# Performance work log

Hardware: AMD Instinct MI355X
Metric: run time of the kernel (lower is better)

The kernel has to match this reference:

```python
import jax, jax.numpy as jnp
import numpy as np

N_KNN = 16
BN_EPS = 1e-5


def conv1d(x, w, b):
    # x: (B,Cin,N), w: (Cout,Cin) -> (B,Cout,N)
    return jnp.einsum('oc,bcn->bon', w, x) + b[None, :, None]


def conv2d(x, w, b):
    # x: (B,Cin,N,K), w: (Cout,Cin) -> (B,Cout,N,K)
    return jnp.einsum('oc,bcnk->bonk', w, x) + b[None, :, None, None]


def bn2d(x, gamma, beta):
    # training-mode BatchNorm2d over (B,N,K) per channel
    mu = x.mean(axis=(0, 2, 3), keepdims=True)
    var = x.var(axis=(0, 2, 3), keepdims=True)
    return (x - mu) * jax.lax.rsqrt(var + BN_EPS) * gamma[None, :, None, None] + beta[None, :, None, None]


def knn_idx(pos, k):
    # pos: (B,3,N) -> (B,N,K) indices of k nearest neighbors (include_self=True)
    p = jnp.transpose(pos, (0, 2, 1))  # (B,N,3)
    sq = jnp.sum(p * p, axis=-1)  # (B,N)
    d = sq[:, :, None] + sq[:, None, :] - 2.0 * jnp.einsum('bnd,bmd->bnm', p, p)
    _, idx = jax.lax.top_k(-d, k)
    return idx


def group(feat, idx):
    # feat: (B,C,N), idx: (B,N,K) -> (B,C,N,K)
    return jnp.take_along_axis(feat[:, :, :, None], idx[:, None, :, :], axis=2)


def mlp_res(x, w1, b1, w2, b2, wsc, bsc):
    shortcut = conv1d(x, wsc, bsc)
    return conv1d(jax.nn.relu(conv1d(x, w1, b1)), w2, b2) + shortcut


def setup_inputs() -> dict:
    key0 = jax.random.key(0)
    ks = jax.random.split(key0, 16)
    B, N, C, D, PH = 2, 2048, 128, 256, 64
    AH = D * 4
    f = lambda i, shape: jax.random.normal(ks[i], shape, jnp.float32) * 0.02
    return dict(
        pos=jax.random.normal(ks[0], (B, 3, N), jnp.float32),
        key=jax.random.normal(ks[1], (B, C, N), jnp.float32),
        query=jax.random.normal(ks[2], (B, C, N), jnp.float32),
        mlp_w1=f(3, (C, 2 * C)), mlp_b1=jnp.zeros(C),
        mlp_w2=f(4, (C, C)), mlp_b2=jnp.zeros(C),
        mlp_wsc=f(5, (C, 2 * C)), mlp_bsc=jnp.zeros(C),
        wk=f(6, (D, C)), bk=jnp.zeros(D),
        wq=f(7, (D, C)), bq=jnp.zeros(D),
        wv=f(8, (D, C)), bv=jnp.zeros(D),
        pos_w1=f(9, (PH, 3)), pos_b1=jnp.zeros(PH),
        pos_g=jnp.ones(PH), pos_beta=jnp.zeros(PH),
        pos_w2=f(10, (D, PH)), pos_b2=jnp.zeros(D),
        attn_w1=f(11, (AH, D)), attn_b1=jnp.zeros(AH),
        attn_g=jnp.ones(AH), attn_beta=jnp.zeros(AH),
        attn_w2=f(12, (D, AH)), attn_b2=jnp.zeros(D),
        end_w=f(13, (C, D)), end_b=jnp.zeros(C),
    )


def reference(pos, key, query,
              mlp_w1, mlp_b1, mlp_w2, mlp_b2, mlp_wsc, mlp_bsc,
              wk, bk, wq, bq, wv, bv,
              pos_w1, pos_b1, pos_g, pos_beta, pos_w2, pos_b2,
              attn_w1, attn_b1, attn_g, attn_beta, attn_w2, attn_b2,
              end_w, end_b):
    # value = MLP_Res(cat(key, query))
    value = mlp_res(jnp.concatenate([key, query], axis=1),
                    mlp_w1, mlp_b1, mlp_w2, mlp_b2, mlp_wsc, mlp_bsc)
    identity = value
    k = conv1d(key, wk, bk)      # (B,D,N)
    q = conv1d(query, wq, bq)    # (B,D,N)
    v = conv1d(value, wv, bv)    # (B,D,N)

    idx = knn_idx(pos, N_KNN)    # (B,N,K)
    key_g = group(k, idx)        # (B,D,N,K)
    qk_rel = q[:, :, :, None] - key_g
    pos_rel = pos[:, :, :, None] - group(pos, idx)  # (B,3,N,K)

    # pos_mlp: conv2d -> BN -> ReLU -> conv2d
    h = jax.nn.relu(bn2d(conv2d(pos_rel, pos_w1, pos_b1), pos_g, pos_beta))
    pos_emb = conv2d(h, pos_w2, pos_b2)  # (B,D,N,K)

    # attn_mlp: conv2d -> BN -> ReLU -> conv2d, softmax over neighbor axis
    a = jax.nn.relu(bn2d(conv2d(qk_rel + pos_emb, attn_w1, attn_b1), attn_g, attn_beta))
    attn = jax.nn.softmax(conv2d(a, attn_w2, attn_b2), axis=-1)  # (B,D,N,K)

    val = v[:, :, :, None] + pos_emb
    agg = jnp.sum(attn * val, axis=-1)  # (B,D,N)
    y = conv1d(agg, end_w, end_b)
    return y + identity
```

## Files before the change

kernel.cpp:

```cpp
#include <hip/hip_runtime.h>
#include <hip/hip_bf16.h>
#include <math.h>

#define Bv 2
#define Nv 2048
#define Cv 128
#define Dv 256
#define PHv 64
#define AHv 1024
#define Kv 16
#define NSAMP (Bv*Nv*Kv)

typedef unsigned short ushortt;
typedef unsigned char u8;
typedef __attribute__((ext_vector_type(8))) short bf16x8;
typedef __attribute__((ext_vector_type(4))) float f32x4;

__device__ __forceinline__ float bf2f(ushortt h){
  union { unsigned int u; float f; } v; v.u = ((unsigned int)h) << 16; return v.f;
}
__device__ __forceinline__ ushortt f2bf(float f){
  union { unsigned int u; float f; } v; v.f = f;
  unsigned int r = v.u + 0x7FFFu + ((v.u >> 16) & 1u);
  return (ushortt)(r >> 16);
}
__device__ __forceinline__ u8 f2fp8(float f){
  union { float f; unsigned int u; } v; v.f = f;
  unsigned int s = (v.u >> 24) & 0x80u;
  unsigned int a = v.u & 0x7FFFFFFFu;
  if (a > 0x43E00000u) a = 0x43E00000u;
  unsigned int r = a + 0x7FFFFu + ((a >> 20) & 1u);
  int e = (int)((r >> 23) & 0xFF) - 120;
  unsigned int m = (r >> 20) & 7u;
  if (e <= 0) return (u8)s;
  return (u8)(s | ((unsigned)e << 3) | m);
}
__device__ __forceinline__ u8 f2fp8u(float f){
  union { float f; unsigned int u; } v; v.f = f;
  unsigned int a = v.u;
  if (a > 0x43E00000u) a = 0x43E00000u;
  unsigned int r = a + 0x7FFFFu + ((a >> 20) & 1u);
  unsigned int out = (r >> 20) - 960u;
  return (u8)(r < 0x3C800000u ? 0u : out);
}

__device__ __forceinline__ void gload16(const void* g, void* l){
  __builtin_amdgcn_global_load_lds(
      (const __attribute__((address_space(1))) unsigned int*)g,
      (__attribute__((address_space(3))) unsigned int*)l, 16, 0, 0);
}

__global__ __launch_bounds__(256) void prep_kernel(
    const float* __restrict__ wk, const float* __restrict__ wq,
    const float* __restrict__ wv, const float* __restrict__ endw,
    const float* __restrict__ mw1, const float* __restrict__ mw2,
    const float* __restrict__ mwsc, const float* __restrict__ aw2,
    const float* __restrict__ pw2,
    const float* __restrict__ key, const float* __restrict__ query,
    ushortt* __restrict__ wA16, ushortt* __restrict__ wB16, ushortt* __restrict__ wv16,
    float* __restrict__ endwT, u8* __restrict__ w2f8, ushortt* __restrict__ pw2R,
    ushortt* __restrict__ hx16)
{
  __shared__ float xs[256*33];
  int t = threadIdx.x;
  if (blockIdx.x < 128){
    int tile = blockIdx.x & 63, b = blockIdx.x >> 6;
    int n0 = tile*32;
    for (int e = t; e < 256*32; e += 256){
      int c = e >> 5, nn = e & 31;
      xs[c*33+nn] = (c < 128) ? key[(size_t)(b*128+c)*Nv + n0+nn]
                              : query[(size_t)(b*128+(c-128))*Nv + n0+nn];
    }
    __syncthreads();
    int nn = t & 31, cg = t >> 5;
    size_t s = (size_t)b*Nv + n0 + nn;
    __align__(16) ushortt tmp[32];
    #pragma unroll
    for (int cc = 0; cc < 32; cc++) tmp[cc] = f2bf(xs[(cg*32+cc)*33 + nn]);
    uint4* dst = (uint4*)&hx16[s*384 + 128 + cg*32];
    #pragma unroll
    for (int q = 0; q < 4; q++) dst[q] = ((uint4*)tmp)[q];
    return;
  }
  int tid = (blockIdx.x-128)*256 + t;
  int stride = (gridDim.x-128)*256;
  for (int i = tid; i < 768*256; i += stride){
    int r = i >> 8, c = i & 255;
    float v;
    if (r < 128) v = mw1[r*256 + c];
    else if (r < 384) v = (c < 128) ? wk[(r-128)*128 + c] : 0.f;
    else if (r < 640) v = (c >= 128) ? wq[(r-384)*128 + (c-128)] : 0.f;
    else v = 0.f;
    wA16[i] = f2bf(v);
  }
  for (int i = tid; i < 128*384; i += stride){
    int r = i / 384, c = i - r*384;
    float v = (c < 128) ? mw2[r*128 + c] : mwsc[r*256 + (c-128)];
    wB16[i] = f2bf(v);
  }
  for (int i = tid; i < 256*128; i += stride) wv16[i] = f2bf(wv[i]);
  for (int i = tid; i < 128*256; i += stride){ int co = i>>8, d = i&255; endwT[d*128+co] = endw[i]; }
  for (int i = tid; i < 256*1024; i += stride) w2f8[i] = f2fp8(aw2[i]*256.f);
  for (int i = tid; i < 256*64; i += stride) pw2R[i] = f2bf(pw2[i]);
}

__global__ __launch_bounds__(512) void gemmA_kernel(
    ushortt* __restrict__ hx16, const ushortt* __restrict__ wA16,
    const float* __restrict__ mb1, const float* __restrict__ bk, const float* __restrict__ bq,
    float* __restrict__ kT, float* __restrict__ qT)
{
  __shared__ ushortt As[128*64];
  __shared__ ushortt Bs[256*64];
  int t = threadIdx.x;
  int w = t >> 6, l = t & 63;
  int lr = l & 15, g4 = l >> 4;
  int wm = w >> 2, wn = w & 3;
  int s0 = blockIdx.x*128, n0 = blockIdx.y*256;

  f32x4 acc[4][4];
  #pragma unroll
  for (int i=0;i<4;i++) for (int j=0;j<4;j++) acc[i][j] = (f32x4){0.f,0.f,0.f,0.f};

  for (int kt = 0; kt < 4; kt++){
    int k0 = kt*64;
    __syncthreads();
    #pragma unroll
    for (int i = 0; i < 2; i++){
      int c = t + i*512;
      int r = c >> 3, db = (c & 7)*16;
      const ushortt* src = hx16 + (size_t)(s0+r)*384 + 128 + k0 + ((db ^ ((r&7)<<4))>>1);
      gload16(src, As + c*8);
    }
    #pragma unroll
    for (int i = 0; i < 4; i++){
      int c = t + i*512;
      int r = c >> 3, db = (c & 7)*16;
      const ushortt* src = wA16 + (size_t)(n0+r)*256 + k0 + ((db ^ ((r&7)<<4))>>1);
      gload16(src, Bs + c*8);
    }
    __syncthreads();
    #pragma unroll
    for (int kk = 0; kk < 2; kk++){
      int kb = kk*64 + g4*16;
      bf16x8 af[4];
      #pragma unroll
      for (int mi = 0; mi < 4; mi++){
        int row = wm*64 + mi*16 + lr;
        af[mi] = *(const bf16x8*)((const char*)As + row*128 + (kb ^ ((row&7)<<4)));
      }
      #pragma unroll
      for (int ni = 0; ni < 4; ni++){
        int row = wn*64 + ni*16 + lr;
        bf16x8 bfr = *(const bf16x8*)((const char*)Bs + row*128 + (kb ^ ((row&7)<<4)));
        #pragma unroll
        for (int mi = 0; mi < 4; mi++)
          acc[mi][ni] = __builtin_amdgcn_mfma_f32_16x16x32_bf16(af[mi], bfr, acc[mi][ni], 0,0,0);
      }
    }
  }
  #pragma unroll
  for (int ni = 0; ni < 4; ni++){
    int col = n0 + wn*64 + ni*16 + lr;
    if (col < 128){
      float bias = mb1[col];
      #pragma unroll
      for (int mi = 0; mi < 4; mi++){
        int rbase = s0 + wm*64 + mi*16 + g4*4;
        #pragma unroll
        for (int r = 0; r < 4; r++){
          float v = acc[mi][ni][r] + bias;
          v = v > 0.f ? v : 0.f;
          hx16[(size_t)(rbase+r)*384 + col] = f2bf(v);
        }
      }
    } else if (col < 384){
      float bias = bk[col-128];
      #pragma unroll
      for (int mi = 0; mi < 4; mi++){
        int rbase = s0 + wm*64 + mi*16 + g4*4;
        #pragma unroll
        for (int r = 0; r < 4; r++)
          kT[(size_t)(rbase+r)*256 + (col-128)] = acc[mi][ni][r] + bias;
      }
    } else if (col < 640){
      float bias = bq[col-384];
      #pragma unroll
      for (int mi = 0; mi < 4; mi++){
        int rbase = s0 + wm*64 + mi*16 + g4*4;
        #pragma unroll
        for (int r = 0; r < 4; r++)
          qT[(size_t)(rbase+r)*256 + (col-384)] = acc[mi][ni][r] + bias;
      }
    }
  }
}

__global__ __launch_bounds__(512) void gemmBC_kernel(
    const ushortt* __restrict__ hx16, const ushortt* __restrict__ wB16,
    const float* __restrict__ mb2, const float* __restrict__ mbsc,
    const ushortt* __restrict__ wv16, const float* __restrict__ bv,
    float* __restrict__ valueT, float* __restrict__ vT)
{
  __shared__ char arena[65536];
  ushortt* As = (ushortt*)arena;
  ushortt* Bs = (ushortt*)(arena + 16384);
  ushortt* Ws = (ushortt*)arena;
  char*    Vs = arena + 32768;
  int t = threadIdx.x;
  int w = t >> 6, l = t & 63;
  int lr = l & 15, g4 = l >> 4;
  int wm = w >> 2, wn = w & 3;
  int s0 = blockIdx.x*128;

  {
    f32x4 acc[4][2];
    #pragma unroll
    for (int i=0;i<4;i++) for (int j=0;j<2;j++) acc[i][j] = (f32x4){0.f,0.f,0.f,0.f};

    for (int kt = 0; kt < 6; kt++){
      int k0 = kt*64;
      __syncthreads();
      #pragma unroll
      for (int i = 0; i < 2; i++){
        int c = t + i*512;
        int r = c >> 3, db = (c & 7)*16;
        const ushortt* src = hx16 + (size_t)(s0+r)*384 + k0 + ((db ^ ((r&7)<<4))>>1);
        gload16(src, As + c*8);
      }
      #pragma unroll
      for (int i = 0; i < 2; i++){
        int c = t + i*512;
        int r = c >> 3, db = (c & 7)*16;
        const ushortt* src = wB16 + (size_t)r*384 + k0 + ((db ^ ((r&7)<<4))>>1);
        gload16(src, Bs + c*8);
      }
      __syncthreads();
      #pragma unroll
      for (int kk = 0; kk < 2; kk++){
        int kb = kk*64 + g4*16;
        bf16x8 af[4];
        #pragma unroll
        for (int mi = 0; mi < 4; mi++){
          int row = wm*64 + mi*16 + lr;
          af[mi] = *(const bf16x8*)((const char*)As + row*128 + (kb ^ ((row&7)<<4)));
        }
        #pragma unroll
        for (int ni = 0; ni < 2; ni++){
          int row = wn*32 + ni*16 + lr;
          bf16x8 bfr = *(const bf16x8*)((const char*)Bs + row*128 + (kb ^ ((row&7)<<4)));
          #pragma unroll
          for (int mi = 0; mi < 4; mi++)
            acc[mi][ni] = __builtin_amdgcn_mfma_f32_16x16x32_bf16(af[mi], bfr, acc[mi][ni], 0,0,0);
        }
      }
    }
    #pragma unroll
    for (int ni = 0; ni < 2; ni++){
      int col = wn*32 + ni*16 + lr;
      float bias = mb2[col] + mbsc[col];
      #pragma unroll
      for (int mi = 0; mi < 4; mi++){
        int rloc = wm*64 + mi*16 + g4*4;
        #pragma unroll
        for (int r = 0; r < 4; r++){
          float v = acc[mi][ni][r] + bias;
          valueT[(size_t)(s0+rloc+r)*128 + col] = v;
          int row = rloc + r;
          *(ushortt*)(Vs + row*256 + ((col*2) ^ ((row&7)<<4))) = f2bf(v);
        }
      }
    }
  }
  {
    f32x4 acc2[4][4];
    #pragma unroll
    for (int i=0;i<4;i++) for (int j=0;j<4;j++) acc2[i][j] = (f32x4){0.f,0.f,0.f,0.f};

    for (int kt = 0; kt < 2; kt++){
      int k0 = kt*64;
      __syncthreads();
      #pragma unroll
      for (int i = 0; i < 4; i++){
        int c = t + i*512;
        int r = c >> 3, db = (c & 7)*16;
        const ushortt* src = wv16 + (size_t)r*128 + k0 + ((db ^ ((r&7)<<4))>>1);
        gload16(src, Ws + c*8);
      }
      __syncthreads();
      #pragma unroll
      for (int kk = 0; kk < 2; kk++){
        int kb = kk*64 + g4*16;
        bf16x8 af[4];
        #pragma unroll
        for (int mi = 0; mi < 4; mi++){
          int row = wm*64 + mi*16 + lr;
          af[mi] = *(const bf16x8*)(Vs + row*256 + ((kt*128 + kb) ^ ((row&7)<<4)));
        }
        #pragma unroll
        for (int ni = 0; ni < 4; ni++){
          int row = wn*64 + ni*16 + lr;
          bf16x8 bfr = *(const bf16x8*)((const char*)Ws + row*128 + (kb ^ ((row&7)<<4)));
          #pragma unroll
          for (int mi = 0; mi < 4; mi++)
            acc2[mi][ni] = __builtin_amdgcn_mfma_f32_16x16x32_bf16(af[mi], bfr, acc2[mi][ni], 0,0,0);
        }
      }
    }
    #pragma unroll
    for (int ni = 0; ni < 4; ni++){
      int col = wn*64 + ni*16 + lr;
      float bias = bv[col];
      #pragma unroll
      for (int mi = 0; mi < 4; mi++){
        int rbase = s0 + wm*64 + mi*16 + g4*4;
        #pragma unroll
        for (int r = 0; r < 4; r++)
          vT[(size_t)(rbase+r)*256 + col] = acc2[mi][ni][r] + bias;
      }
    }
  }
}

__global__ __launch_bounds__(256) void knn_kernel(const float* __restrict__ pos, int* __restrict__ idx)
{
  int t = threadIdx.x;
  int w = t >> 6, l = t & 63;
  int p = blockIdx.x*4 + w;
  int i = p & (Nv-1), b = p >> 11;
  const float* px = pos + (size_t)b*3*Nv;
  float pix = px[i], piy = px[Nv+i], piz = px[2*Nv+i];
  float sqi = pix*pix + piy*piy + piz*piz;
  float ds[32];
  #pragma unroll
  for (int jj = 0; jj < 32; jj++){
    int j = jj*64 + l;
    float qx = px[j], qy = px[Nv+j], qz = px[2*Nv+j];
    float sqj = qx*qx + qy*qy + qz*qz;
    float dot = pix*qx + piy*qy + piz*qz;
    ds[jj] = (sqi + sqj) - 2.0f*dot;
  }
  #pragma unroll 1
  for (int it = 0; it < 16; it++){
    float bv = 3.4e38f; int bj = 0x7FFFFFFF;
    #pragma unroll
    for (int jj = 0; jj < 32; jj++){
      int j = jj*64 + l;
      bool c = ds[jj] < bv;
      bv = c ? ds[jj] : bv;
      bj = c ? j : bj;
    }
    #pragma unroll
    for (int off = 32; off; off >>= 1){
      float ov = __shfl_xor(bv, off);
      int oj = __shfl_xor(bj, off);
      if (ov < bv || (ov == bv && oj < bj)){ bv = ov; bj = oj; }
    }
    if (l == 0) idx[(size_t)p*16 + it] = bj;
    #pragma unroll
    for (int jj = 0; jj < 32; jj++){
      if (jj*64 + l == bj) ds[jj] = 3.4e38f;
    }
  }
}

__global__ __launch_bounds__(256) void bn1_stats(const float* __restrict__ pos,
    const int* __restrict__ idx, float* __restrict__ rstat)
{
  int tid = blockIdx.x*256 + threadIdx.x;
  int stride = gridDim.x*256;
  float s[9] = {0,0,0,0,0,0,0,0,0};
  for (int e = tid; e < NSAMP; e += stride){
    int b = e >> 15;
    int rem = e & 32767;
    int n = rem >> 4, k = rem & 15;
    int j = idx[(size_t)(b*Nv+n)*16 + k];
    const float* px = pos + (size_t)b*3*Nv;
    float rx = px[n]-px[j], ry = px[Nv+n]-px[Nv+j], rz = px[2*Nv+n]-px[2*Nv+j];
    s[0]+=rx; s[1]+=ry; s[2]+=rz;
    s[3]+=rx*rx; s[4]+=rx*ry; s[5]+=rx*rz; s[6]+=ry*ry; s[7]+=ry*rz; s[8]+=rz*rz;
  }
  for (int off=32; off; off>>=1)
    for (int q=0;q<9;q++) s[q] += __shfl_xor(s[q], off);
  if ((threadIdx.x & 63) == 0)
    for (int q=0;q<9;q++) atomicAdd(&rstat[q], s[q]);
}

__global__ __launch_bounds__(256) void hpos_kernel(
    const float* __restrict__ pos, const int* __restrict__ idx,
    const float* __restrict__ rstat, const float* __restrict__ pw1,
    const float* __restrict__ pg, const float* __restrict__ pbeta,
    ushortt* __restrict__ hposR)
{
  __shared__ float w1s[192];
  __shared__ float b1s[64];
  int t = threadIdx.x;
  if (t < 64){
    float inv = 1.0f/(float)NSAMP;
    float mux = rstat[0]*inv, muy = rstat[1]*inv, muz = rstat[2]*inv;
    float xx = rstat[3]*inv, xy = rstat[4]*inv, xz = rstat[5]*inv;
    float yy = rstat[6]*inv, yz = rstat[7]*inv, zz = rstat[8]*inv;
    float w0 = pw1[t*3], w1 = pw1[t*3+1], w2 = pw1[t*3+2];
    float dot = w0*mux + w1*muy + w2*muz;
    float quad = w0*w0*xx + w1*w1*yy + w2*w2*zz + 2.f*(w0*w1*xy + w0*w2*xz + w1*w2*yz);
    float var = quad - dot*dot;
    float sc = pg[t] * rsqrtf(var + 1e-5f);
    w1s[t*3]   = w0*sc;
    w1s[t*3+1] = w1*sc;
    w1s[t*3+2] = w2*sc;
    b1s[t] = pbeta[t] - dot*sc;
  }
  __syncthreads();
  int s = blockIdx.x*32 + (t>>3);
  int c0 = (t&7)*8;
  int ptv = s >> 4;
  int n = ptv & (Nv-1), b = ptv >> 11;
  int j = idx[s];
  const float* px = pos + (size_t)b*3*Nv;
  float rx = px[n]-px[j], ry = px[Nv+n]-px[Nv+j], rz = px[2*Nv+n]-px[2*Nv+j];
  ushortt outv[8];
  #pragma unroll
  for (int e = 0; e < 8; e++){
    int c = c0+e;
    float v = b1s[c] + w1s[c*3]*rx + w1s[c*3+1]*ry + w1s[c*3+2]*rz;
    outv[e] = f2bf(v > 0.f ? v : 0.f);
  }
  *(uint4*)&hposR[(size_t)s*64 + c0] = *(uint4*)outv;
}

__global__ __launch_bounds__(512) void gemm0_kernel(
    const ushortt* __restrict__ hposR, const ushortt* __restrict__ pw2R,
    const float* __restrict__ pb2, const int* __restrict__ idx,
    const float* __restrict__ qT, const float* __restrict__ kT, const float* __restrict__ vT,
    ushortt* __restrict__ U16, ushortt* __restrict__ val16, float* __restrict__ mu_sum)
{
  __shared__ ushortt As[128*64];
  __shared__ ushortt Bs[256*64];
  __shared__ float mured[8*256];
  int t = threadIdx.x;
  int w = t >> 6, l = t & 63;
  int lr = l & 15, g4 = l >> 4;
  int wm = w >> 2, wn = w & 3;
  int s0 = blockIdx.x*128;

  #pragma unroll
  for (int i = 0; i < 2; i++){
    int c = t + i*512;
    int r = c >> 3, db = (c & 7)*16;
    const ushortt* src = hposR + (size_t)(s0+r)*64 + ((db ^ ((r&7)<<4))>>1);
    gload16(src, As + c*8);
  }
  #pragma unroll
  for (int i = 0; i < 4; i++){
    int c = t + i*512;
    int r = c >> 3, db = (c & 7)*16;
    const ushortt* src = pw2R + (size_t)r*64 + ((db ^ ((r&7)<<4))>>1);
    gload16(src, Bs + c*8);
  }
  __syncthreads();

  f32x4 acc[4][4];
  #pragma unroll
  for (int i=0;i<4;i++) for (int j=0;j<4;j++) acc[i][j] = (f32x4){0.f,0.f,0.f,0.f};
  #pragma unroll
  for (int kk = 0; kk < 2; kk++){
    int kb = kk*64 + g4*16;
    bf16x8 af[4];
    #pragma unroll
    for (int mi = 0; mi < 4; mi++){
      int row = wm*64 + mi*16 + lr;
      af[mi] = *(const bf16x8*)((const char*)As + row*128 + (kb ^ ((row&7)<<4)));
    }
    #pragma unroll
    for (int ni = 0; ni < 4; ni++){
      int row = wn*64 + ni*16 + lr;
      bf16x8 bfr = *(const bf16x8*)((const char*)Bs + row*128 + (kb ^ ((row&7)<<4)));
      #pragma unroll
      for (int mi = 0; mi < 4; mi++)
        acc[mi][ni] = __builtin_amdgcn_mfma_f32_16x16x32_bf16(af[mi], bfr, acc[mi][ni], 0,0,0);
    }
  }

  float musum[4] = {0.f,0.f,0.f,0.f};
  __align__(16) float pb2v[4];
  #pragma unroll
  for (int ni = 0; ni < 4; ni++) pb2v[ni] = pb2[wn*64 + ni*16 + lr];
  #pragma unroll
  for (int mi = 0; mi < 4; mi++){
    #pragma unroll
    for (int r4 = 0; r4 < 4; r4++){
      int s = s0 + wm*64 + mi*16 + g4*4 + r4;
      int ptv = s >> 4;
      int b = s >> 15;
      int j = idx[s];
      const float* krow = kT + (size_t)(b*Nv + j)*256;
      const float* qrow = qT + (size_t)ptv*256;
      const float* vrow = vT + (size_t)ptv*256;
      #pragma unroll
      for (int ni = 0; ni < 4; ni++){
        int d = wn*64 + ni*16 + lr;
        float pe = acc[mi][ni][r4] + pb2v[ni];
        float u = qrow[d] - krow[d] + pe;
        U16[(size_t)s*256 + d] = f2bf(u);
        val16[(size_t)s*256 + d] = f2bf(vrow[d] + pe);
        musum[ni] += u;
      }
    }
  }
  #pragma unroll
  for (int ni = 0; ni < 4; ni++)
    mured[(wm*4+g4)*256 + wn*64 + ni*16 + lr] = musum[ni];
  __syncthreads();
  if (t < 256){
    float ssum = 0.f;
    #pragma unroll
    for (int q = 0; q < 8; q++) ssum += mured[q*256 + t];
    atomicAdd(&mu_sum[t], ssum);
  }
}

__global__ __launch_bounds__(512) void mm_kernel(const ushortt* __restrict__ U16,
                                                 ushortt* __restrict__ Mpart)
{
  __shared__ ushortt Ut[256*64];
  int t = threadIdx.x;
  int w = t >> 6, l = t & 63;
  int lr = l & 15, g4 = l >> 4;
  int wm = w >> 2, wn = w & 3;
  int c_my = ((w & 3)*64 + l);
  int sg = w >> 2;
  int blk = blockIdx.x;
  int sstart = blk*256;

  f32x4 acc[8][4];
  #pragma unroll
  for (int i=0;i<8;i++) for (int j=0;j<4;j++) acc[i][j] = (f32x4){0.f,0.f,0.f,0.f};

  for (int st = 0; st < 4; st++){
    int sb = sstart + st*64;
    __syncthreads();
    #pragma unroll
    for (int g = 0; g < 4; g++){
      int s8 = sg*32 + g*8;
      ushortt vals[8];
      #pragma unroll
      for (int e = 0; e < 8; e++)
        vals[e] = U16[(size_t)(sb + s8 + e)*256 + c_my];
      unsigned int p0 = (unsigned int)vals[0] | ((unsigned int)vals[1] << 16);
      unsigned int p1 = (unsigned int)vals[2] | ((unsigned int)vals[3] << 16);
      unsigned int p2 = (unsigned int)vals[4] | ((unsigned int)vals[5] << 16);
      unsigned int p3 = (unsigned int)vals[6] | ((unsigned int)vals[7] << 16);
      uint4 pk = make_uint4(p0,p1,p2,p3);
      *(uint4*)((char*)Ut + c_my*128 + ((s8*2) ^ ((c_my&7)<<4))) = pk;
    }
    __syncthreads();
    #pragma unroll
    for (int kk = 0; kk < 2; kk++){
      int kb = kk*64 + g4*16;
      bf16x8 af[8];
      #pragma unroll
      for (int ci = 0; ci < 8; ci++){
        int row = wm*128 + ci*16 + lr;
        af[ci] = *(const bf16x8*)((const char*)Ut + row*128 + (kb ^ ((row&7)<<4)));
      }
      #pragma unroll
      for (int cj = 0; cj < 4; cj++){
        int row = wn*64 + cj*16 + lr;
        bf16x8 bfr = *(const bf16x8*)((const char*)Ut + row*128 + (kb ^ ((row&7)<<4)));
        #pragma unroll
        for (int ci = 0; ci < 8; ci++)
          acc[ci][cj] = __builtin_amdgcn_mfma_f32_16x16x32_bf16(af[ci], bfr, acc[ci][cj], 0,0,0);
      }
    }
  }
  ushortt* dst = Mpart + (size_t)blk*65536;
  #pragma unroll
  for (int ci = 0; ci < 8; ci++){
    #pragma unroll
    for (int cj = 0; cj < 4; cj++){
      int c2 = wn*64 + cj*16 + lr;
      #pragma unroll
      for (int r = 0; r < 4; r++){
        int c1 = wm*128 + ci*16 + g4*4 + r;
        dst[(size_t)c1*256 + c2] = f2bf(acc[ci][cj][r]);
      }
    }
  }
}

__global__ __launch_bounds__(256) void mreduce_kernel(const ushortt* __restrict__ Mpart,
                                                      float* __restrict__ Mm)
{
  int i = blockIdx.x*256 + threadIdx.x;
  float s = 0.f;
  for (int p = 0; p < 256; p++) s += bf2f(Mpart[(size_t)p*65536 + i]);
  Mm[i] = s;
}

__global__ __launch_bounds__(256) void bn2_final(
    const float* __restrict__ Mm, const float* __restrict__ mu_sum,
    const float* __restrict__ aw1,
    const float* __restrict__ ag, const float* __restrict__ abeta,
    ushortt* __restrict__ w1R, float* __restrict__ b1eff2)
{
  __shared__ float wrow[256];
  __shared__ float red[8];
  __shared__ float s2s;
  int t = threadIdx.x;
  int ch = blockIdx.x;
  wrow[t] = aw1[(size_t)ch*256 + t];
  __syncthreads();
  float colacc = 0.f;
  for (int r = 0; r < 256; r++) colacc += wrow[r] * Mm[(size_t)r*256 + t];
  float inv = 1.0f/(float)NSAMP;
  float qpart = colacc * wrow[t] * inv;
  float dpart = wrow[t] * mu_sum[t] * inv;
  for (int off=32; off; off>>=1){ qpart += __shfl_xor(qpart, off); dpart += __shfl_xor(dpart, off); }
  if ((t&63)==0){ red[t>>6] = qpart; red[4 + (t>>6)] = dpart; }
  __syncthreads();
  if (t == 0){
    float quad = red[0]+red[1]+red[2]+red[3];
    float dot  = red[4]+red[5]+red[6]+red[7];
    float var = quad - dot*dot;
    float s2 = ag[ch] * rsqrtf(var + 1e-5f);
    b1eff2[ch] = abeta[ch] - dot*s2;
    s2s = s2;
  }
  __syncthreads();
  w1R[(size_t)ch*256 + t] = f2bf(wrow[t]*s2s);
}

__global__ __launch_bounds__(512) void gemm1_kernel(
    const ushortt* __restrict__ U16c, const ushortt* __restrict__ w1R,
    const float* __restrict__ b1eff2, u8* __restrict__ H)
{
  __shared__ ushortt As[128*64];
  __shared__ ushortt Bs[256*64];
  int t = threadIdx.x;
  int w = t >> 6, l = t & 63;
  int lr = l & 15, g4 = l >> 4;
  int wm = w >> 2, wn = w & 3;
  int nwg = gridDim.x, cpx = nwg >> 3;
  int logical = (blockIdx.x & 7)*cpx + (blockIdx.x >> 3);
  int mt = logical >> 2, nt = logical & 3;
  int s0 = mt*128, n0 = nt*256;

  f32x4 acc[4][4];
  #pragma unroll
  for (int i=0;i<4;i++) for (int j=0;j<4;j++) acc[i][j] = (f32x4){0.f,0.f,0.f,0.f};

  for (int kt = 0; kt < 4; kt++){
    int k0 = kt*64;
    __syncthreads();
    #pragma unroll
    for (int i = 0; i < 2; i++){
      int c = t + i*512;
      int r = c >> 3, db = (c & 7)*16;
      const ushortt* src = U16c + (size_t)(s0+r)*256 + k0 + ((db ^ ((r&7)<<4))>>1);
      gload16(src, As + c*8);
    }
    #pragma unroll
    for (int i = 0; i < 4; i++){
      int c = t + i*512;
      int r = c >> 3, db = (c & 7)*16;
      const ushortt* src = w1R + (size_t)(n0+r)*256 + k0 + ((db ^ ((r&7)<<4))>>1);
      gload16(src, Bs + c*8);
    }
    __syncthreads();
    #pragma unroll
    for (int kk = 0; kk < 2; kk++){
      int kb = kk*64 + g4*16;
      bf16x8 af[4];
      #pragma unroll
      for (int mi = 0; mi < 4; mi++){
        int row = wm*64 + mi*16 + lr;
        af[mi] = *(const bf16x8*)((const char*)As + row*128 + (kb ^ ((row&7)<<4)));
      }
      #pragma unroll
      for (int ni = 0; ni < 4; ni++){
        int row = wn*64 + ni*16 + lr;
        bf16x8 bfr = *(const bf16x8*)((const char*)Bs + row*128 + (kb ^ ((row&7)<<4)));
        #pragma unroll
        for (int mi = 0; mi < 4; mi++)
          acc[mi][ni] = __builtin_amdgcn_mfma_f32_16x16x32_bf16(af[mi], bfr, acc[mi][ni], 0,0,0);
      }
    }
  }
  __syncthreads();
  u8* rep = (u8*)Bs;
  #pragma unroll
  for (int ni = 0; ni < 4; ni++){
    int colc = wn*64 + ni*16 + lr;
    float bias = b1eff2[n0 + colc];
    #pragma unroll
    for (int mi = 0; mi < 4; mi++){
      int sloc = wm*64 + mi*16 + g4*4;
      #pragma unroll
      for (int r = 0; r < 4; r++){
        float v = acc[mi][ni][r] + bias;
        v = v > 0.f ? v : 0.f;
        rep[(sloc+r)*256 + colc] = f2fp8u(4.f*v);
      }
    }
  }
  __syncthreads();
  #pragma unroll
  for (int i = 0; i < 4; i++){
    int e = t + i*512;
    int row = e >> 4, off = (e & 15)*16;
    *(uint4*)&H[(size_t)(s0+row)*1024 + n0 + off] = *(const uint4*)(rep + e*16);
  }
}

__global__ __launch_bounds__(512) void gemm2_kernel(
    const u8* __restrict__ H, const u8* __restrict__ w2f8,
    const float* __restrict__ ab2, const ushortt* __restrict__ val16,
    float* __restrict__ aggT, int s_off)
{
  __shared__ u8 As8[128*128];
  __shared__ u8 Bs8[256*128];
  int t = threadIdx.x;
  int w = t >> 6, l = t & 63;
  int lr = l & 15, g4 = l >> 4;
  int wm = w >> 2, wn = w & 3;
  int blk = blockIdx.x;
  int s0 = blk*128;

  f32x4 acc[4][4];
  #pragma unroll
  for (int i=0;i<4;i++) for (int j=0;j<4;j++) acc[i][j] = (f32x4){0.f,0.f,0.f,0.f};

  for (int kt = 0; kt < 8; kt++){
    int k0 = kt*128;
    __syncthreads();
    #pragma unroll
    for (int i = 0; i < 2; i++){
      int c = t + i*512;
      int r = c >> 3, db = (c & 7)*16;
      const u8* src = H + (size_t)(s0+r)*1024 + k0 + (db ^ ((r&7)<<4));
      gload16(src, As8 + c*16);
    }
    #pragma unroll
    for (int i = 0; i < 4; i++){
      int c = t + i*512;
      int r = c >> 3, db = (c & 7)*16;
      const u8* src = w2f8 + (size_t)r*1024 + k0 + (db ^ ((r&7)<<4));
      gload16(src, Bs8 + c*16);
    }
    __syncthreads();
    #pragma unroll
    for (int kk = 0; kk < 4; kk++){
      int kb = kk*32 + g4*8;
      long af[4];
      #pragma unroll
      for (int mi = 0; mi < 4; mi++){
        int row = wm*64 + mi*16 + lr;
        af[mi] = *(const long*)(As8 + row*128 + (kb ^ ((row&7)<<4)));
      }
      #pragma unroll
      for (int ni = 0; ni < 4; ni++){
        int row = wn*64 + ni*16 + lr;
        long bfr = *(const long*)(Bs8 + row*128 + (kb ^ ((row&7)<<4)));
        #pragma unroll
        for (int mi = 0; mi < 4; mi++)
          acc[mi][ni] = __builtin_amdgcn_mfma_f32_16x16x32_fp8_fp8(af[mi], bfr, acc[mi][ni], 0,0,0);
      }
    }
  }
  const float sc = 1.0f/1024.0f;
  int ptbase = s_off >> 4;
  #pragma unroll
  for (int mi = 0; mi < 4; mi++){
    int pt = ptbase + blk*8 + wm*4 + mi;
    int sbase = pt*16;
    #pragma unroll
    for (int ni = 0; ni < 4; ni++){
      int d = wn*64 + ni*16 + lr;
      float bias = ab2[d];
      float lg[4];
      #pragma unroll
      for (int r = 0; r < 4; r++) lg[r] = acc[mi][ni][r]*sc + bias;
      float mx = fmaxf(fmaxf(lg[0],lg[1]), fmaxf(lg[2],lg[3]));
      mx = fmaxf(mx, __shfl_xor(mx, 16));
      mx = fmaxf(mx, __shfl_xor(mx, 32));
      float ev[4], ss = 0.f;
      #pragma unroll
      for (int r = 0; r < 4; r++){ ev[r] = __expf(lg[r]-mx); ss += ev[r]; }
      ss += __shfl_xor(ss, 16);
      ss += __shfl_xor(ss, 32);
      float inv = 1.0f/ss;
      float pa = 0.f;
      #pragma unroll
      for (int r = 0; r < 4; r++){
        int s = sbase + g4*4 + r;
        pa += ev[r]*inv*bf2f(val16[(size_t)s*256 + d]);
      }
      pa += __shfl_xor(pa, 16);
      pa += __shfl_xor(pa, 32);
      if (g4 == 0) aggT[(size_t)pt*256 + d] = pa;
    }
  }
}

__global__ __launch_bounds__(256) void final_kernel(
    const float* __restrict__ aggT, const float* __restrict__ endwT,
    const float* __restrict__ endb, const float* __restrict__ valueT,
    float* __restrict__ out)
{
  __shared__ float ags[32*257];
  int t = threadIdx.x;
  int tile = blockIdx.x & 63, b = blockIdx.x >> 6;
  int n0 = tile*32;
  for (int e = t; e < 32*256; e += 256){
    int nn = e >> 8, d = e & 255;
    ags[nn*257 + d] = aggT[(size_t)(b*Nv + n0 + nn)*256 + d];
  }
  __syncthreads();
  int cg = t >> 2, ng = t & 3;
  int co0 = cg*2, nb = ng*8;
  float acc[2][8];
  for (int i=0;i<2;i++){ float bb = endb[co0+i]; for (int j=0;j<8;j++) acc[i][j]=bb; }
  for (int d = 0; d < 256; d++){
    float w0 = endwT[d*128 + co0], w1 = endwT[d*128 + co0 + 1];
    #pragma unroll
    for (int j=0;j<8;j++){
      float av = ags[(nb+j)*257 + d];
      acc[0][j] += w0*av; acc[1][j] += w1*av;
    }
  }
  for (int i=0;i<2;i++){
    for (int j=0;j<8;j++){
      int n = n0 + nb + j;
      size_t o = (size_t)(b*128 + co0 + i)*Nv + n;
      out[o] = acc[i][j] + valueT[(size_t)(b*Nv + n)*128 + co0 + i];
    }
  }
}

extern "C" void kernel_launch(void* const* d_in, const int* in_sizes, int n_in,
                              void* d_out, int out_size, void* d_ws, size_t ws_size,
                              hipStream_t stream)
{
  (void)in_sizes; (void)n_in; (void)out_size;
  const float* pos   = (const float*)d_in[0];
  const float* key   = (const float*)d_in[1];
  const float* query = (const float*)d_in[2];
  const float* mw1   = (const float*)d_in[3];
  const float* mb1   = (const float*)d_in[4];
  const float* mw2   = (const float*)d_in[5];
  const float* mb2   = (const float*)d_in[6];
  const float* mwsc  = (const float*)d_in[7];
  const float* mbsc  = (const float*)d_in[8];
  const float* wk    = (const float*)d_in[9];
  const float* bk    = (const float*)d_in[10];
  const float* wq    = (const float*)d_in[11];
  const float* bq    = (const float*)d_in[12];
  const float* wv    = (const float*)d_in[13];
  const float* bv    = (const float*)d_in[14];
  const float* pw1   = (const float*)d_in[15];
  const float* pg    = (const float*)d_in[17];
  const float* pbeta = (const float*)d_in[18];
  const float* pw2   = (const float*)d_in[19];
  const float* pb2   = (const float*)d_in[20];
  const float* aw1   = (const float*)d_in[21];
  const float* ag    = (const float*)d_in[23];
  const float* abeta = (const float*)d_in[24];
  const float* aw2   = (const float*)d_in[25];
  const float* ab2   = (const float*)d_in[26];
  const float* endw  = (const float*)d_in[27];
  const float* endb  = (const float*)d_in[28];
  float* out = (float*)d_out;

  char* wsb = (char*)d_ws;
  size_t off = 0;
  auto take = [&](size_t bytes)->char*{
    char* p = wsb + off; off += (bytes + 255) & ~(size_t)255; return p;
  };
  float* Mm      = (float*)take(65536*4);
  float* mu_sum  = (float*)take(256*4);
  float* rstat   = (float*)take(12*4);
  size_t zero_bytes = off;
  float* b1eff2  = (float*)take(1024*4);
  float* valueT  = (float*)take((size_t)524288*4);
  float* qT      = (float*)take((size_t)1048576*4);
  float* kT      = (float*)take((size_t)1048576*4);
  float* vT      = (float*)take((size_t)1048576*4);
  float* aggT    = (float*)take((size_t)1048576*4);
  float* endwT   = (float*)take(32768*4);
  int*   idxb    = (int*)take(65536*4);
  ushortt* hx16  = (ushortt*)take((size_t)4096*384*2);
  ushortt* wA16  = (ushortt*)take((size_t)768*256*2);
  ushortt* wB16  = (ushortt*)take((size_t)128*384*2);
  ushortt* wv16  = (ushortt*)take((size_t)256*128*2);
  ushortt* U16   = (ushortt*)take((size_t)16777216*2);
  ushortt* val16 = (ushortt*)take((size_t)16777216*2);
  ushortt* hposR = (ushortt*)take((size_t)4194304*2);
  ushortt* Mpart = (ushortt*)take((size_t)256*65536*2);
  ushortt* w1R   = (ushortt*)take((size_t)262144*2);
  u8*      w2f8  = (u8*)take((size_t)262144);
  ushortt* pw2R  = (ushortt*)take(16384*2);

  size_t avail = (ws_size > off) ? (ws_size - off) : 0;
  int nch = 1;
  while (nch < 64 && ((size_t)(NSAMP/nch))*1024 > avail) nch <<= 1;
  int chunk = NSAMP / nch;
  u8* H = (u8*)(wsb + off);

  hipMemsetAsync(d_ws, 0, zero_bytes, stream);
  prep_kernel<<<640,256,0,stream>>>(wk,wq,wv,endw,mw1,mw2,mwsc,aw2,pw2,key,query,
                                    wA16,wB16,wv16,endwT,w2f8,pw2R,hx16);
  knn_kernel<<<1024,256,0,stream>>>(pos,idxb);
  gemmA_kernel<<<dim3(32,3),512,0,stream>>>(hx16,wA16,mb1,bk,bq,kT,qT);
  gemmBC_kernel<<<32,512,0,stream>>>(hx16,wB16,mb2,mbsc,wv16,bv,valueT,vT);
  bn1_stats<<<64,256,0,stream>>>(pos,idxb,rstat);
  hpos_kernel<<<2048,256,0,stream>>>(pos,idxb,rstat,pw1,pg,pbeta,hposR);
  gemm0_kernel<<<512,512,0,stream>>>(hposR,pw2R,pb2,idxb,qT,kT,vT,U16,val16,mu_sum);
  mm_kernel<<<256,512,0,stream>>>(U16,Mpart);
  mreduce_kernel<<<256,256,0,stream>>>(Mpart,Mm);
  bn2_final<<<1024,256,0,stream>>>(Mm,mu_sum,aw1,ag,abeta,w1R,b1eff2);
  for (int cc = 0; cc < nch; cc++){
    int s_off = cc*chunk;
    gemm1_kernel<<<(chunk/128)*4,512,0,stream>>>(U16 + (size_t)s_off*256, w1R, b1eff2, H);
    gemm2_kernel<<<chunk/128,512,0,stream>>>(H, w2f8, ab2, val16, aggT, s_off);
  }
  final_kernel<<<128,256,0,stream>>>(aggT,endwT,endb,valueT,out);
}
```

Baseline: 280.9 us.

## Fuse attention MLP GEMM1 and GEMM2 keeping hidden activations in LDS

Merges the two attention-MLP GEMMs into one kernel. Each block computes its 128-sample hidden tile in 256-column chunks, quantizes it to fp8 in shared memory, and feeds it straight into the second GEMM with the softmax/aggregation epilogue. This removes the large fp8 H round trip through global memory and the chunked launch loop. In exchange, each block recomputes over all four N tiles serially, so there is less parallelism per launch (512 blocks instead of 2048+512) and shared memory use grows to 64KB, which lowers occupancy.

New measurement: 357.7 us. 27.3% more time.

```diff
diff --git a/kernel.cpp b/kernel.cpp
--- a/kernel.cpp
+++ b/kernel.cpp
@@ -629,148 +629,123 @@
   w1R[(size_t)ch*256 + t] = f2bf(wrow[t]*s2s);
 }
 
-__global__ __launch_bounds__(512) void gemm1_kernel(
-    const ushortt* __restrict__ U16c, const ushortt* __restrict__ w1R,
-    const float* __restrict__ b1eff2, u8* __restrict__ H)
-{
-  __shared__ ushortt As[128*64];
-  __shared__ ushortt Bs[256*64];
+__global__ __launch_bounds__(512) void gemm12_kernel(
+    const ushortt* __restrict__ U16, const ushortt* __restrict__ w1R,
+    const float* __restrict__ b1eff2, const u8* __restrict__ w2f8,
+    const float* __restrict__ ab2, const ushortt* __restrict__ val16,
+    float* __restrict__ aggT)
+{
+  __shared__ char arena[65536];
+  ushortt* As  = (ushortt*)arena;
+  ushortt* Bs1 = (ushortt*)(arena + 16384);
+  u8* Hs  = (u8*)arena;
+  u8* W2s = (u8*)(arena + 32768);
   int t = threadIdx.x;
   int w = t >> 6, l = t & 63;
   int lr = l & 15, g4 = l >> 4;
   int wm = w >> 2, wn = w & 3;
   int nwg = gridDim.x, cpx = nwg >> 3;
-  int logical = (blockIdx.x & 7)*cpx + (blockIdx.x >> 3);
-  int mt = logical >> 2, nt = logical & 3;
-  int s0 = mt*128, n0 = nt*256;
-
-  f32x4 acc[4][4];
-  #pragma unroll
-  for (int i=0;i<4;i++) for (int j=0;j<4;j++) acc[i][j] = (f32x4){0.f,0.f,0.f,0.f};
-
-  for (int kt = 0; kt < 4; kt++){
-    int k0 = kt*64;
+  int mt = (blockIdx.x & 7)*cpx + (blockIdx.x >> 3);
+  int s0 = mt*128;
+
+  f32x4 acc2[4][4];
+  #pragma unroll
+  for (int i=0;i<4;i++) for (int j=0;j<4;j++) acc2[i][j] = (f32x4){0.f,0.f,0.f,0.f};
+
+  for (int nt = 0; nt < 4; nt++){
+    int n0 = nt*256;
+    f32x4 acc1[4][4];
+    #pragma unroll
+    for (int i=0;i<4;i++) for (int j=0;j<4;j++) acc1[i][j] = (f32x4){0.f,0.f,0.f,0.f};
+    for (int kt = 0; kt < 4; kt++){
+      int k0 = kt*64;
+      __syncthreads();
+      #pragma unroll
+      for (int i = 0; i < 2; i++){
+        int c = t + i*512;
+        int r = c >> 3, db = (c & 7)*16;
+        const ushortt* src = U16 + (size_t)(s0+r)*256 + k0 + ((db ^ ((r&7)<<4))>>1);
+        gload16(src, As + c*8);
+      }
+      #pragma unroll
+      for (int i = 0; i < 4; i++){
+        int c = t + i*512;
+        int r = c >> 3, db = (c & 7)*16;
+        const ushortt* src = w1R + (size_t)(n0+r)*256 + k0 + ((db ^ ((r&7)<<4))>>1);
+        gload16(src, Bs1 + c*8);
+      }
+      __syncthreads();
+      #pragma unroll
+      for (int kk = 0; kk < 2; kk++){
+        int kb = kk*64 + g4*16;
+        bf16x8 af[4];
+        #pragma unroll
+        for (int mi = 0; mi < 4; mi++){
+          int row = wm*64 + mi*16 + lr;
+          af[mi] = *(const bf16x8*)((const char*)As + row*128 + (kb ^ ((row&7)<<4)));
+        }
+        #pragma unroll
+        for (int ni = 0; ni < 4; ni++){
+          int row = wn*64 + ni*16 + lr;
+          bf16x8 bfr = *(const bf16x8*)((const char*)Bs1 + row*128 + (kb ^ ((row&7)<<4)));
+          #pragma unroll
+          for (int mi = 0; mi < 4; mi++)
+            acc1[mi][ni] = __builtin_amdgcn_mfma_f32_16x16x32_bf16(af[mi], bfr, acc1[mi][ni], 0,0,0);
+        }
+      }
+    }
     __syncthreads();
     #pragma unroll
-    for (int i = 0; i < 2; i++){
-      int c = t + i*512;
-      int r = c >> 3, db = (c & 7)*16;
-      const ushortt* src = U16c + (size_t)(s0+r)*256 + k0 + ((db ^ ((r&7)<<4))>>1);
-      gload16(src, As + c*8);
-    }
-    #pragma unroll
-    for (int i = 0; i < 4; i++){
-      int c = t + i*512;
-      int r = c >> 3, db = (c & 7)*16;
-      const ushortt* src = w1R + (size_t)(n0+r)*256 + k0 + ((db ^ ((r&7)<<4))>>1);
-      gload16(src, Bs + c*8);
-    }
-    __syncthreads();
-    #pragma unroll
-    for (int kk = 0; kk < 2; kk++){
-      int kb = kk*64 + g4*16;
-      bf16x8 af[4];
+    for (int ni = 0; ni < 4; ni++){
+      int colc = wn*64 + ni*16 + lr;
+      float bias = b1eff2[n0 + colc];
       #pragma unroll
       for (int mi = 0; mi < 4; mi++){
-        int row = wm*64 + mi*16 + lr;
-        af[mi] = *(const bf16x8*)((const char*)As + row*128 + (kb ^ ((row&7)<<4)));
-      }
-      #pragma unroll
-      for (int ni = 0; ni < 4; ni++){
-        int row = wn*64 + ni*16 + lr;
-        bf16x8 bfr = *(const bf16x8*)((const char*)Bs + row*128 + (kb ^ ((row&7)<<4)));
-        #pragma unroll
-        for (int mi = 0; mi < 4; mi++)
-          acc[mi][ni] = __builtin_amdgcn_mfma_f32_16x16x32_bf16(af[mi], bfr, acc[mi][ni], 0,0,0);
-      }
-    }
-  }
-  __syncthreads();
-  u8* rep = (u8*)Bs;
-  #pragma unroll
-  for (int ni = 0; ni < 4; ni++){
-    int colc = wn*64 + ni*16 + lr;
-    float bias = b1eff2[n0 + colc];
-    #pragma unroll
-    for (int mi = 0; mi < 4; mi++){
-      int sloc = wm*64 + mi*16 + g4*4;
-      #pragma unroll
-      for (int r = 0; r < 4; r++){
-        float v = acc[mi][ni][r] + bias;
-        v = v > 0.f ? v : 0.f;
-        rep[(sloc+r)*256 + colc] = f2fp8u(4.f*v);
-      }
-    }
-  }
-  __syncthreads();
-  #pragma unroll
-  for (int i = 0; i < 4; i++){
-    int e = t + i*512;
-    int row = e >> 4, off = (e & 15)*16;
-    *(uint4*)&H[(size_t)(s0+row)*1024 + n0 + off] = *(const uint4*)(rep + e*16);
-  }
-}
-
-__global__ __launch_bounds__(512) void gemm2_kernel(
-    const u8* __restrict__ H, const u8* __restrict__ w2f8,
-    const float* __restrict__ ab2, const ushortt* __restrict__ val16,
-    float* __restrict__ aggT, int s_off)
-{
-  __shared__ u8 As8[128*128];
-  __shared__ u8 Bs8[256*128];
-  int t = threadIdx.x;
-  int w = t >> 6, l = t & 63;
-  int lr = l & 15, g4 = l >> 4;
-  int wm = w >> 2, wn = w & 3;
-  int blk = blockIdx.x;
-  int s0 = blk*128;
-
-  f32x4 acc[4][4];
-  #pragma unroll
-  for (int i=0;i<4;i++) for (int j=0;j<4;j++) acc[i][j] = (f32x4){0.f,0.f,0.f,0.f};
-
-  for (int kt = 0; kt < 8; kt++){
-    int k0 = kt*128;
-    __syncthreads();
-    #pragma unroll
-    for (int i = 0; i < 2; i++){
-      int c = t + i*512;
-      int r = c >> 3, db = (c & 7)*16;
-      const u8* src = H + (size_t)(s0+r)*1024 + k0 + (db ^ ((r&7)<<4));
-      gload16(src, As8 + c*16);
-    }
-    #pragma unroll
-    for (int i = 0; i < 4; i++){
-      int c = t + i*512;
-      int r = c >> 3, db = (c & 7)*16;
-      const u8* src = w2f8 + (size_t)r*1024 + k0 + (db ^ ((r&7)<<4));
-      gload16(src, Bs8 + c*16);
-    }
-    __syncthreads();
-    #pragma unroll
-    for (int kk = 0; kk < 4; kk++){
-      int kb = kk*32 + g4*8;
-      long af[4];
-      #pragma unroll
-      for (int mi = 0; mi < 4; mi++){
-        int row = wm*64 + mi*16 + lr;
-        af[mi] = *(const long*)(As8 + row*128 + (kb ^ ((row&7)<<4)));
-      }
-      #pragma unroll
-      for (int ni = 0; ni < 4; ni++){
-        int row = wn*64 + ni*16 + lr;
-        long bfr = *(const long*)(Bs8 + row*128 + (kb ^ ((row&7)<<4)));
-        #pragma unroll
-        for (int mi = 0; mi < 4; mi++)
-          acc[mi][ni] = __builtin_amdgcn_mfma_f32_16x16x32_fp8_fp8(af[mi], bfr, acc[mi][ni], 0,0,0);
-      }
+        int sloc = wm*64 + mi*16 + g4*4;
+        #pragma unroll
+        for (int r = 0; r < 4; r++){
+          float v = acc1[mi][ni][r] + bias;
+          v = v > 0.f ? v : 0.f;
+          int row = sloc + r;
+          Hs[row*256 + (colc ^ ((row&7)<<4))] = f2fp8u(4.f*v);
+        }
+      }
+    }
+    #pragma unroll
+    for (int sub = 0; sub < 2; sub++){
+      #pragma unroll
+      for (int i = 0; i < 4; i++){
+        int c = t + i*512;
+        int r = c >> 3, db = (c & 7)*16;
+        const u8* src = w2f8 + (size_t)r*1024 + n0 + sub*128 + (db ^ ((r&7)<<4));
+        gload16(src, W2s + c*16);
+      }
+      __syncthreads();
+      #pragma unroll
+      for (int kk = 0; kk < 4; kk++){
+        int kb = kk*32 + g4*8;
+        long af[4];
+        #pragma unroll
+        for (int mi = 0; mi < 4; mi++){
+          int row = wm*64 + mi*16 + lr;
+          af[mi] = *(const long*)(Hs + row*256 + ((sub*128 + kb) ^ ((row&7)<<4)));
+        }
+        #pragma unroll
+        for (int ni = 0; ni < 4; ni++){
+          int row = wn*64 + ni*16 + lr;
+          long bfr = *(const long*)(W2s + row*128 + (kb ^ ((row&7)<<4)));
+          #pragma unroll
+          for (int mi = 0; mi < 4; mi++)
+            acc2[mi][ni] = __builtin_amdgcn_mfma_f32_16x16x32_fp8_fp8(af[mi], bfr, acc2[mi][ni], 0,0,0);
+        }
+      }
+      __syncthreads();
     }
   }
   const float sc = 1.0f/1024.0f;
-  int ptbase = s_off >> 4;
   #pragma unroll
   for (int mi = 0; mi < 4; mi++){
-    int pt = ptbase + blk*8 + wm*4 + mi;
+    int pt = mt*8 + wm*4 + mi;
     int sbase = pt*16;
     #pragma unroll
     for (int ni = 0; ni < 4; ni++){
@@ -778,7 +753,7 @@
       float bias = ab2[d];
       float lg[4];
       #pragma unroll
-      for (int r = 0; r < 4; r++) lg[r] = acc[mi][ni][r]*sc + bias;
+      for (int r = 0; r < 4; r++) lg[r] = acc2[mi][ni][r]*sc + bias;
       float mx = fmaxf(fmaxf(lg[0],lg[1]), fmaxf(lg[2],lg[3]));
       mx = fmaxf(mx, __shfl_xor(mx, 16));
       mx = fmaxf(mx, __shfl_xor(mx, 32));
@@ -840,7 +815,7 @@
                               void* d_out, int out_size, void* d_ws, size_t ws_size,
                               hipStream_t stream)
 {
-  (void)in_sizes; (void)n_in; (void)out_size;
+  (void)in_sizes; (void)n_in; (void)out_size; (void)ws_size;
   const float* pos   = (const float*)d_in[0];
   const float* key   = (const float*)d_in[1];
   const float* query = (const float*)d_in[2];
@@ -899,12 +874,6 @@
   u8*      w2f8  = (u8*)take((size_t)262144);
   ushortt* pw2R  = (ushortt*)take(16384*2);
 
-  size_t avail = (ws_size > off) ? (ws_size - off) : 0;
-  int nch = 1;
-  while (nch < 64 && ((size_t)(NSAMP/nch))*1024 > avail) nch <<= 1;
-  int chunk = NSAMP / nch;
-  u8* H = (u8*)(wsb + off);
-
   hipMemsetAsync(d_ws, 0, zero_bytes, stream);
   prep_kernel<<<640,256,0,stream>>>(wk,wq,wv,endw,mw1,mw2,mwsc,aw2,pw2,key,query,
                                     wA16,wB16,wv16,endwT,w2f8,pw2R,hx16);
@@ -917,10 +886,6 @@
   mm_kernel<<<256,512,0,stream>>>(U16,Mpart);
   mreduce_kernel<<<256,256,0,stream>>>(Mpart,Mm);
   bn2_final<<<1024,256,0,stream>>>(Mm,mu_sum,aw1,ag,abeta,w1R,b1eff2);
-  for (int cc = 0; cc < nch; cc++){
-    int s_off = cc*chunk;
-    gemm1_kernel<<<(chunk/128)*4,512,0,stream>>>(U16 + (size_t)s_off*256, w1R, b1eff2, H);
-    gemm2_kernel<<<chunk/128,512,0,stream>>>(H, w2f8, ab2, val16, aggT, s_off);
-  }
+  gemm12_kernel<<<512,512,0,stream>>>(U16,w1R,b1eff2,w2f8,ab2,val16,aggT);
   final_kernel<<<128,256,0,stream>>>(aggT,endwT,endb,valueT,out);
 }
```
